# Performance work log

Measured on AMD Instinct MI355X. Metric: run time of the kernel, lower is better.

## Reference

```python
import jax, jax.numpy as jnp
import numpy as np

VOCAB = 50257
EMBED = 512
HEADS = 8
HEAD_DIM = EMBED // HEADS
WINDOW = 128
NUM_CLASS = 20
B, S = 4, 2048


def setup_inputs() -> dict:
    key = jax.random.key(0)
    ks = jax.random.split(key, 16)
    sc = 0.02
    inp = {
        'text': jax.random.randint(ks[0], (B, S), 0, VOCAB),
        'emb': jax.random.normal(ks[1], (VOCAB, EMBED), jnp.float32) * sc,
        'in_w': jax.random.normal(ks[2], (3 * EMBED, EMBED), jnp.float32) * sc,
        'in_b': jnp.zeros((3 * EMBED,), jnp.float32),
        'out_w': jax.random.normal(ks[3], (EMBED, EMBED), jnp.float32) * sc,
        'out_b': jnp.zeros((EMBED,), jnp.float32),
        'w1': jax.random.normal(ks[4], (512, EMBED), jnp.float32) * sc,
        'b1': jnp.zeros((512,), jnp.float32),
        'w2': jax.random.normal(ks[5], (256, 512), jnp.float32) * sc,
        'b2': jnp.zeros((256,), jnp.float32),
        'w3': jax.random.normal(ks[6], (128, 256), jnp.float32) * sc,
        'b3': jnp.zeros((128,), jnp.float32),
        'w4': jax.random.normal(ks[7], (NUM_CLASS, 128), jnp.float32) * sc,
        'b4': jnp.zeros((NUM_CLASS,), jnp.float32),
    }
    return inp


def _banded_mask(seq_len, window):
    i = jnp.arange(seq_len)[:, None]
    j = jnp.arange(seq_len)[None, :]
    allowed = jnp.abs(i - j) <= window  # band of width 2*window+1
    return jnp.where(allowed, 0.0, -jnp.inf).astype(jnp.float32)


def reference(text, emb, in_w, in_b, out_w, out_b, w1, b1, w2, b2, w3, b3, w4, b4):
    # Embedding lookup (dropout is identity in eval mode)
    x = emb[text]  # [B, S, E]
    b, s, e = x.shape

    # torch nn.MultiheadAttention: packed in_proj, scaling by 1/sqrt(head_dim)
    wq, wk, wv = in_w[:e], in_w[e:2 * e], in_w[2 * e:]
    bq, bk, bv = in_b[:e], in_b[e:2 * e], in_b[2 * e:]
    q = (x @ wq.T + bq).reshape(b, s, HEADS, HEAD_DIM)
    k = (x @ wk.T + bk).reshape(b, s, HEADS, HEAD_DIM)
    v = (x @ wv.T + bv).reshape(b, s, HEADS, HEAD_DIM)

    mask = _banded_mask(s, WINDOW)  # [S, S] additive, -inf outside band
    scores = jnp.einsum('bihd,bjhd->bhij', q, k) / jnp.sqrt(jnp.float32(HEAD_DIM))
    probs = jax.nn.softmax(scores + mask, axis=-1)  # [B, H, S, S]
    attn = jnp.einsum('bhij,bjhd->bihd', probs, v).reshape(b, s, e)
    attn = attn @ out_w.T + out_b  # [B, S, E]

    # max-pool over sequence
    ctx = jnp.max(attn, axis=1)  # [B, E]

    # MLP head with leaky_relu (negative_slope=0.01, torch default)
    h = jax.nn.leaky_relu(ctx @ w1.T + b1, 0.01)
    h = jax.nn.leaky_relu(h @ w2.T + b2, 0.01)
    h = jax.nn.leaky_relu(h @ w3.T + b3, 0.01)
    return h @ w4.T + b4  # [B, NUM_CLASS]
```

## Files before the change

kernel.cpp:

```cpp
#include <hip/hip_runtime.h>

typedef unsigned short u16;
typedef __attribute__((ext_vector_type(8))) short bf16x8;
typedef __attribute__((ext_vector_type(4))) float f32x4;

#define S_LEN 2048
#define EMBED 512
#define HEADS 8
#define HDIM 64
#define BATCH 4
#define TOKENS (BATCH * S_LEN)

__device__ __forceinline__ u16 f2bf(float f) {
  union { float f; unsigned u; } v;
  v.f = f;
  unsigned r = v.u + 0x7fffu + ((v.u >> 16) & 1u);
  return (u16)(r >> 16);
}

__device__ __forceinline__ unsigned fkey(float f) {
  unsigned u = __float_as_uint(f);
  return (u & 0x80000000u) ? ~u : (u | 0x80000000u);
}
__device__ __forceinline__ float funkey(unsigned k) {
  unsigned u = (k & 0x80000000u) ? (k ^ 0x80000000u) : ~k;
  return __uint_as_float(u);
}

__device__ __forceinline__ void gl2lds16(const void* g, void* l) {
  __builtin_amdgcn_global_load_lds(
      (const __attribute__((address_space(1))) void*)g,
      (__attribute__((address_space(3))) void*)l, 16, 0, 0);
}

__global__ __launch_bounds__(256) void prep_kernel(
    const int* __restrict__ text, const float* __restrict__ emb,
    const float* __restrict__ in_w, const float* __restrict__ out_w,
    u16* __restrict__ Xb, u16* __restrict__ Wq, u16* __restrict__ Wo,
    unsigned* __restrict__ ctxi) {
  const int bid = blockIdx.x;
  const int tid = threadIdx.x;
  if (bid < 1024) {
    const int t = bid * 8 + (tid >> 5);
    const int c0 = (tid & 31) * 16;
    const float* src = emb + (size_t)text[t] * EMBED + c0;
    u16* dst = Xb + (size_t)t * EMBED + c0;
#pragma unroll
    for (int j = 0; j < 4; ++j) {
      const float4 v = *(const float4*)(src + j * 4);
      dst[j * 4 + 0] = f2bf(v.x); dst[j * 4 + 1] = f2bf(v.y);
      dst[j * 4 + 2] = f2bf(v.z); dst[j * 4 + 3] = f2bf(v.w);
    }
  } else if (bid < 1152) {
    const int wb = bid - 1024;
#pragma unroll
    for (int j = 0; j < 8; ++j) {
      const int idx4 = wb * 2048 + j * 256 + tid;
      const int idx = idx4 * 4;
      const float* src;
      u16* dst;
      if (idx < 1536 * 512) { src = in_w + idx; dst = Wq + idx; }
      else { src = out_w + (idx - 1536 * 512); dst = Wo + (idx - 1536 * 512); }
      const float4 v = *(const float4*)src;
      dst[0] = f2bf(v.x); dst[1] = f2bf(v.y); dst[2] = f2bf(v.z); dst[3] = f2bf(v.w);
    }
  } else {
    for (int i = tid; i < BATCH * EMBED; i += 256) ctxi[i] = 0u;
  }
}

__global__ __launch_bounds__(256, 3) void qkv_mfma(
    const u16* __restrict__ Xb, const u16* __restrict__ Wq,
    const float* __restrict__ in_b,
    u16* __restrict__ qg, u16* __restrict__ kg, u16* __restrict__ vt) {
  __shared__ u16 SM[16384];
  u16* const As = SM;
  u16* const Bs = SM + 8192;
  const int lid = blockIdx.x;
  const int xcd = lid & 7, idx = lid >> 3;
  const int m0 = (xcd * 8 + idx / 12) * 128;
  const int n0 = (idx % 12) * 128;
  const int tid = threadIdx.x;
  const int w = tid >> 6, l = tid & 63, quad = l >> 4, ln = l & 15;
  const int rb = (w >> 1) * 64, cb = (w & 1) * 64;

  f32x4 acc[4][4] = {};

  for (int k0 = 0; k0 < EMBED; k0 += 64) {
#pragma unroll
    for (int it = 0; it < 4; ++it) {
      const int chunk = it * 256 + tid;
      const int row = chunk >> 3, cp = chunk & 7, c = cp ^ (row & 7);
      gl2lds16(Xb + (size_t)(m0 + row) * EMBED + k0 + c * 8, &As[chunk * 8]);
      gl2lds16(Wq + (size_t)(n0 + row) * EMBED + k0 + c * 8, &Bs[chunk * 8]);
    }
    __syncthreads();
#pragma unroll
    for (int s = 0; s < 2; ++s) {
      bf16x8 af[4], bf[4];
#pragma unroll
      for (int i = 0; i < 4; ++i) {
        const int r = rb + 16 * i + ln;
        af[i] = *(const bf16x8*)&As[r * 64 + (((s << 2) + quad) ^ (r & 7)) * 8];
      }
#pragma unroll
      for (int j = 0; j < 4; ++j) {
        const int n = cb + 16 * j + ln;
        bf[j] = *(const bf16x8*)&Bs[n * 64 + (((s << 2) + quad) ^ (n & 7)) * 8];
      }
#pragma unroll
      for (int i = 0; i < 4; ++i)
#pragma unroll
        for (int j = 0; j < 4; ++j)
          acc[i][j] = __builtin_amdgcn_mfma_f32_16x16x32_bf16(af[i], bf[j], acc[i][j], 0, 0, 0);
    }
    __syncthreads();
  }

  const int b = m0 >> 11;
  if (n0 < 1024) {
#pragma unroll
    for (int j = 0; j < 4; ++j) {
      const int n = n0 + cb + 16 * j + ln;
      const float bias = in_b[n];
      const int sec = n >> 9, f = n & 511, h = f >> 6, d = f & 63;
#pragma unroll
      for (int i = 0; i < 4; ++i) {
#pragma unroll
        for (int r = 0; r < 4; ++r) {
          const int t = m0 + rb + 16 * i + quad * 4 + r;
          const int s = t & 2047;
          const float val = acc[i][j][r] + bias;
          if (sec == 0)
            qg[((size_t)((b * HEADS + h) * S_LEN + s)) * HDIM + d] = f2bf(val * 0.125f);
          else
            kg[((size_t)((b * HEADS + h) * S_LEN + s)) * HDIM + d] = f2bf(val);
        }
      }
    }
  } else {
#pragma unroll
    for (int j = 0; j < 4; ++j) {
      const int col = cb + 16 * j + ln;
      const float bias = in_b[n0 + col];
#pragma unroll
      for (int i = 0; i < 4; ++i) {
#pragma unroll
        for (int r = 0; r < 4; ++r) {
          const int row = rb + 16 * i + quad * 4 + r;
          SM[row * 128 + (col ^ (((row >> 3) & 3) << 4))] = f2bf(acc[i][j][r] + bias);
        }
      }
    }
    __syncthreads();
#pragma unroll
    for (int itd = 0; itd < 2; ++itd) {
      const int dl = w * 32 + itd * 16 + ln;
      const int f = (n0 + dl) & 511, h = f >> 6, d = f & 63;
      u16* dst = vt + ((size_t)((b * HEADS + h) * HDIM + d)) * S_LEN + (m0 & 2047);
#pragma unroll
      for (int it2 = 0; it2 < 4; ++it2) {
        const int sb = quad * 8 + it2 * 32;
        const int swc = dl ^ (((sb >> 3) & 3) << 4);
        union { u16 a[8]; bf16x8 v; } u;
#pragma unroll
        for (int k = 0; k < 8; ++k) u.a[k] = SM[(sb + k) * 128 + swc];
        *(bf16x8*)(dst + sb) = u.v;
      }
    }
  }
}

__global__ __launch_bounds__(256, 3) void attn_mfma(
    const u16* __restrict__ qg, const u16* __restrict__ kg,
    const u16* __restrict__ vt, u16* __restrict__ attnb) {
  __shared__ u16 KV[320 * 64];
  __shared__ u16 Pb[4][16 * 40];
  const int lid = blockIdx.x;
  const int nid = (lid & 7) * 128 + (lid >> 3);
  const int bh = nid >> 5;
  const int i0 = (nid & 31) * 64;
  const int jb = i0 - 128;
  const int tid = threadIdx.x;
  const int w = tid >> 6, l = tid & 63, quad = l >> 4, ln = l & 15;

  const u16* qrow = qg + ((size_t)bh * S_LEN + i0 + w * 16 + ln) * HDIM;
  bf16x8 qf[2];
  qf[0] = *(const bf16x8*)(qrow + quad * 8);
  qf[1] = *(const bf16x8*)(qrow + 32 + quad * 8);

  const u16* kbase = kg + (size_t)bh * S_LEN * HDIM;
#pragma unroll
  for (int it = 0; it < 10; ++it) {
    const int chunk = it * 256 + tid;
    const int row = chunk >> 3, cp = chunk & 7, c = cp ^ (row & 7);
    int gj = jb + row;
    gj = gj < 0 ? 0 : (gj > S_LEN - 1 ? S_LEN - 1 : gj);
    gl2lds16(kbase + (size_t)gj * HDIM + c * 8, &KV[chunk * 8]);
  }
  __syncthreads();

  f32x4 sc[18] = {};
#pragma unroll
  for (int jj = 0; jj < 17; ++jj) {
    const int r = (w + jj) * 16 + ln;
    const bf16x8 b0 = *(const bf16x8*)&KV[r * 64 + ((quad) ^ (r & 7)) * 8];
    const bf16x8 b1 = *(const bf16x8*)&KV[r * 64 + ((4 + quad) ^ (r & 7)) * 8];
    f32x4 a = {};
    a = __builtin_amdgcn_mfma_f32_16x16x32_bf16(qf[0], b0, a, 0, 0, 0);
    a = __builtin_amdgcn_mfma_f32_16x16x32_bf16(qf[1], b1, a, 0, 0, 0);
    sc[jj] = a;
  }
  __syncthreads();

  const u16* vbase = vt + (size_t)bh * HDIM * S_LEN;
#pragma unroll
  for (int it = 0; it < 10; ++it) {
    const int chunk = it * 256 + tid;
    const int row = chunk / 40, cp = chunk % 40, c = cp ^ (row & 7);
    int gc = jb + c * 8;
    gc = gc < 0 ? 0 : (gc > S_LEN - 8 ? S_LEN - 8 : gc);
    gl2lds16(vbase + (size_t)row * S_LEN + gc, &KV[chunk * 8]);
  }

  const int q4 = quad * 4;
  float lrow[4] = {0.f, 0.f, 0.f, 0.f};
  const bool interior = (jb >= 0) && (jb + 320 <= S_LEN);
  if (interior) {
#pragma unroll
    for (int jj = 0; jj < 17; ++jj) {
#pragma unroll
      for (int r = 0; r < 4; ++r) {
        const bool valid =
            (jj == 0) ? (q4 + r <= ln) : ((jj == 16) ? (q4 + r >= ln) : true);
        const float e = valid ? __expf(sc[jj][r]) : 0.f;
        sc[jj][r] = e;
        lrow[r] += e;
      }
    }
  } else {
    const int gibase = i0 + w * 16 + q4;
    int lo[4], hi[4];
#pragma unroll
    for (int r = 0; r < 4; ++r) {
      const int gi = gibase + r;
      int lr = gi - 128, hr = gi + 128;
      lo[r] = lr < 0 ? 0 : lr;
      hi[r] = hr > S_LEN - 1 ? S_LEN - 1 : hr;
    }
#pragma unroll
    for (int jj = 0; jj < 17; ++jj) {
      const int gj = jb + (w + jj) * 16 + ln;
#pragma unroll
      for (int r = 0; r < 4; ++r) {
        const bool valid = (gj >= lo[r]) && (gj <= hi[r]);
        const float e = valid ? __expf(sc[jj][r]) : 0.f;
        sc[jj][r] = e;
        lrow[r] += e;
      }
    }
  }
#pragma unroll
  for (int r = 0; r < 4; ++r) {
    lrow[r] += __shfl_xor(lrow[r], 1);
    lrow[r] += __shfl_xor(lrow[r], 2);
    lrow[r] += __shfl_xor(lrow[r], 4);
    lrow[r] += __shfl_xor(lrow[r], 8);
    lrow[r] = 1.0f / lrow[r];
  }

  __syncthreads();

  f32x4 oacc[4] = {};
  u16* pb = &Pb[w][0];
#pragma unroll
  for (int kt = 0; kt < 9; ++kt) {
#pragma unroll
    for (int tt = 0; tt < 2; ++tt) {
      const int s = kt * 2 + tt;
#pragma unroll
      for (int r = 0; r < 4; ++r)
        pb[(q4 + r) * 40 + ln + 16 * tt] = f2bf(sc[s][r]);
    }
    __asm__ volatile("" ::: "memory");
    const bf16x8 pa = *(const bf16x8*)&pb[ln * 40 + quad * 8];
#pragma unroll
    for (int dt = 0; dt < 4; ++dt) {
      const int d = dt * 16 + ln;
      int cc = 2 * w + kt * 4 + quad;
      cc = cc > 39 ? 39 : cc;
      const bf16x8 vb = *(const bf16x8*)&KV[d * 320 + (cc ^ (d & 7)) * 8];
      oacc[dt] = __builtin_amdgcn_mfma_f32_16x16x32_bf16(pa, vb, oacc[dt], 0, 0, 0);
    }
  }

  const int b = bh >> 3, h = bh & 7;
#pragma unroll
  for (int dt = 0; dt < 4; ++dt) {
    const int d = h * HDIM + dt * 16 + ln;
#pragma unroll
    for (int r = 0; r < 4; ++r) {
      const int gi = i0 + w * 16 + q4 + r;
      attnb[((size_t)(b * S_LEN + gi)) * EMBED + d] = f2bf(oacc[dt][r] * lrow[r]);
    }
  }
}

__global__ __launch_bounds__(256, 3) void outproj_mfma(
    const u16* __restrict__ attnb, const u16* __restrict__ Wo,
    const float* __restrict__ out_b, unsigned* __restrict__ ctxi) {
  __shared__ u16 As[128 * 64];
  __shared__ u16 Bs[64 * 64];
  __shared__ float red[4][32];
  const int lid = blockIdx.x;
  const int xcd = lid & 7, idx = lid >> 3;
  const int m0 = (xcd * 8 + (idx >> 3)) * 128;
  const int n0 = (idx & 7) * 64;
  const int tid = threadIdx.x;
  const int w = tid >> 6, l = tid & 63, quad = l >> 4, ln = l & 15;
  const int rb = (w >> 1) * 64, cb = (w & 1) * 32;

  f32x4 acc[4][2] = {};

  for (int k0 = 0; k0 < EMBED; k0 += 64) {
#pragma unroll
    for (int it = 0; it < 4; ++it) {
      const int chunk = it * 256 + tid;
      const int row = chunk >> 3, cp = chunk & 7, c = cp ^ (row & 7);
      gl2lds16(attnb + (size_t)(m0 + row) * EMBED + k0 + c * 8, &As[chunk * 8]);
    }
#pragma unroll
    for (int it = 0; it < 2; ++it) {
      const int chunk = it * 256 + tid;
      const int row = chunk >> 3, cp = chunk & 7, c = cp ^ (row & 7);
      gl2lds16(Wo + (size_t)(n0 + row) * EMBED + k0 + c * 8, &Bs[chunk * 8]);
    }
    __syncthreads();
#pragma unroll
    for (int s = 0; s < 2; ++s) {
      bf16x8 af[4], bf[2];
#pragma unroll
      for (int i = 0; i < 4; ++i) {
        const int r = rb + 16 * i + ln;
        af[i] = *(const bf16x8*)&As[r * 64 + (((s << 2) + quad) ^ (r & 7)) * 8];
      }
#pragma unroll
      for (int j = 0; j < 2; ++j) {
        const int n = cb + 16 * j + ln;
        bf[j] = *(const bf16x8*)&Bs[n * 64 + (((s << 2) + quad) ^ (n & 7)) * 8];
      }
#pragma unroll
      for (int i = 0; i < 4; ++i)
#pragma unroll
        for (int j = 0; j < 2; ++j)
          acc[i][j] = __builtin_amdgcn_mfma_f32_16x16x32_bf16(af[i], bf[j], acc[i][j], 0, 0, 0);
    }
    __syncthreads();
  }

  float cm[2];
#pragma unroll
  for (int j = 0; j < 2; ++j) {
    float m = -1e30f;
#pragma unroll
    for (int i = 0; i < 4; ++i)
#pragma unroll
      for (int r = 0; r < 4; ++r) m = fmaxf(m, acc[i][j][r]);
    m = fmaxf(m, __shfl_xor(m, 16));
    m = fmaxf(m, __shfl_xor(m, 32));
    cm[j] = m;
  }
  if (l < 16) {
#pragma unroll
    for (int j = 0; j < 2; ++j) red[w][16 * j + ln] = cm[j];
  }
  __syncthreads();
  if (tid < 64) {
    const int half = tid >> 5;
    const int cc = tid & 31;
    const float m = fmaxf(red[half][cc], red[half + 2][cc]);
    const int n = n0 + tid;
    const int b = m0 >> 11;
    atomicMax(&ctxi[b * EMBED + n], fkey(m + out_b[n]));
  }
}

__global__ __launch_bounds__(256) void mlp_l1(
    const unsigned* __restrict__ ctxi, const float* __restrict__ w1,
    const float* __restrict__ b1, float* __restrict__ h1g) {
  __shared__ float ctx[512];
  const int b = blockIdx.x >> 5, chunk = blockIdx.x & 31;
  const int tid = threadIdx.x;
  for (int e = tid; e < 512; e += 256) ctx[e] = funkey(ctxi[b * 512 + e]);
  __syncthreads();

  const int og = tid >> 4, ln = tid & 15;
  const int o = chunk * 16 + og;
  const float4* wv = (const float4*)(w1 + (size_t)o * 512 + ln * 32);
  const float4* xv = (const float4*)(ctx + ln * 32);
  float acc = 0.f;
#pragma unroll
  for (int k = 0; k < 8; ++k) {
    const float4 a = wv[k], x = xv[k];
    acc += a.x * x.x + a.y * x.y + a.z * x.z + a.w * x.w;
  }
  acc += __shfl_xor(acc, 1);
  acc += __shfl_xor(acc, 2);
  acc += __shfl_xor(acc, 4);
  acc += __shfl_xor(acc, 8);
  if (ln == 0) {
    const float a = acc + b1[o];
    h1g[b * 512 + o] = a > 0.f ? a : 0.01f * a;
  }
}

__global__ __launch_bounds__(256) void mlp_l2(
    const float* __restrict__ h1g, const float* __restrict__ w2,
    const float* __restrict__ b2, float* __restrict__ h2g) {
  __shared__ float xb[512];
  const int b = blockIdx.x >> 4, chunk = blockIdx.x & 15;
  const int tid = threadIdx.x;
  for (int e = tid; e < 512; e += 256) xb[e] = h1g[b * 512 + e];
  __syncthreads();

  const int og = tid >> 4, ln = tid & 15;
  const int o = chunk * 16 + og;
  const float4* wv = (const float4*)(w2 + (size_t)o * 512 + ln * 32);
  const float4* xv = (const float4*)(xb + ln * 32);
  float acc = 0.f;
#pragma unroll
  for (int k = 0; k < 8; ++k) {
    const float4 a = wv[k], x = xv[k];
    acc += a.x * x.x + a.y * x.y + a.z * x.z + a.w * x.w;
  }
  acc += __shfl_xor(acc, 1);
  acc += __shfl_xor(acc, 2);
  acc += __shfl_xor(acc, 4);
  acc += __shfl_xor(acc, 8);
  if (ln == 0) {
    const float a = acc + b2[o];
    h2g[b * 256 + o] = a > 0.f ? a : 0.01f * a;
  }
}

__global__ __launch_bounds__(256) void mlp_l34(
    const float* __restrict__ h2g,
    const float* __restrict__ w3, const float* __restrict__ b3,
    const float* __restrict__ w4, const float* __restrict__ b4,
    float* __restrict__ out) {
  __shared__ float xb[256], h3[128];
  const int b = blockIdx.x, tid = threadIdx.x;
  if (tid < 256) xb[tid] = h2g[b * 256 + tid];
  __syncthreads();

  {
    const int o = tid >> 1, kh = tid & 1;
    float acc = 0.f;
    const float* wr = w3 + (size_t)o * 256 + kh * 128;
    const float* xr = xb + kh * 128;
    for (int k = 0; k < 128; k += 4) {
      const float4 wv = *(const float4*)(wr + k);
      const float4 xv = *(const float4*)(xr + k);
      acc += wv.x * xv.x + wv.y * xv.y + wv.z * xv.z + wv.w * xv.w;
    }
    acc += __shfl_xor(acc, 1);
    if (kh == 0) { const float a = acc + b3[o]; h3[o] = a > 0.f ? a : 0.01f * a; }
  }
  __syncthreads();

  if (tid < 160) {
    const int o = tid >> 3, ks = tid & 7;
    const float* wr = w4 + (size_t)o * 128 + ks * 16;
    const float* xr = h3 + ks * 16;
    float acc = 0.f;
    for (int k = 0; k < 16; k += 4) {
      const float4 wv = *(const float4*)(wr + k);
      const float4 xv = *(const float4*)(xr + k);
      acc += wv.x * xv.x + wv.y * xv.y + wv.z * xv.z + wv.w * xv.w;
    }
    acc += __shfl_xor(acc, 1);
    acc += __shfl_xor(acc, 2);
    acc += __shfl_xor(acc, 4);
    if (ks == 0) out[b * 20 + o] = acc + b4[o];
  }
}

extern "C" void kernel_launch(void* const* d_in, const int* in_sizes, int n_in,
                              void* d_out, int out_size, void* d_ws, size_t ws_size,
                              hipStream_t stream) {
  (void)in_sizes; (void)n_in; (void)out_size; (void)ws_size;
  const int*   text  = (const int*)d_in[0];
  const float* emb   = (const float*)d_in[1];
  const float* in_w  = (const float*)d_in[2];
  const float* in_b  = (const float*)d_in[3];
  const float* out_w = (const float*)d_in[4];
  const float* out_b = (const float*)d_in[5];
  const float* w1 = (const float*)d_in[6];
  const float* b1 = (const float*)d_in[7];
  const float* w2 = (const float*)d_in[8];
  const float* b2 = (const float*)d_in[9];
  const float* w3 = (const float*)d_in[10];
  const float* b3 = (const float*)d_in[11];
  const float* w4 = (const float*)d_in[12];
  const float* b4 = (const float*)d_in[13];

  char* ws = (char*)d_ws;
  u16* Xb   = (u16*)(ws);
  u16* Wq   = (u16*)(ws + 8388608);
  u16* Wo   = (u16*)(ws + 9961472);
  u16* qg   = (u16*)(ws + 10485760);
  u16* kg   = (u16*)(ws + 18874368);
  u16* vt   = (u16*)(ws + 27262976);
  u16* attn = (u16*)(ws + 35651584);
  unsigned* ctxi = (unsigned*)(ws + 44040192);
  float* h1g  = (float*)(ws + 44048384);
  float* h2g  = (float*)(ws + 44056576);

  prep_kernel<<<1153, 256, 0, stream>>>(text, emb, in_w, out_w, Xb, Wq, Wo, ctxi);
  qkv_mfma<<<768, 256, 0, stream>>>(Xb, Wq, in_b, qg, kg, vt);
  attn_mfma<<<1024, 256, 0, stream>>>(qg, kg, vt, attn);
  outproj_mfma<<<512, 256, 0, stream>>>(attn, Wo, out_b, ctxi);
  mlp_l1<<<128, 256, 0, stream>>>(ctxi, w1, b1, h1g);
  mlp_l2<<<64, 256, 0, stream>>>(h1g, w2, b2, h2g);
  mlp_l34<<<4, 256, 0, stream>>>(h2g, w3, b3, w4, b4, (float*)d_out);
}
```

Baseline: 216.7 us.

## Shrink outproj tile to 64x64 and simplify attention K/V load addressing

The out-projection GEMM moves from 128x64 tiles (each wave computing a 64x32 sub-tile) to 64x64 tiles, where each wave computes a 16x64 strip. This doubles the grid to 1024 blocks and raises the launch-bounds occupancy hint. The attention kernel now skips the index clamping for interior K windows and replaces the per-iteration divide/modulo in the V load with incremental row/column tracking. The smaller tiles give more parallelism and occupancy, but reuse less data per loaded A/B element and emit twice as many atomicMax updates.

```diff
diff --git a/kernel.cpp b/kernel.cpp
--- a/kernel.cpp
+++ b/kernel.cpp
@@ -183,6 +183,7 @@
   const int jb = i0 - 128;
   const int tid = threadIdx.x;
   const int w = tid >> 6, l = tid & 63, quad = l >> 4, ln = l & 15;
+  const bool interior = (jb >= 0) && (jb + 320 <= S_LEN);
 
   const u16* qrow = qg + ((size_t)bh * S_LEN + i0 + w * 16 + ln) * HDIM;
   bf16x8 qf[2];
@@ -190,13 +191,23 @@
   qf[1] = *(const bf16x8*)(qrow + 32 + quad * 8);
 
   const u16* kbase = kg + (size_t)bh * S_LEN * HDIM;
-#pragma unroll
-  for (int it = 0; it < 10; ++it) {
-    const int chunk = it * 256 + tid;
-    const int row = chunk >> 3, cp = chunk & 7, c = cp ^ (row & 7);
-    int gj = jb + row;
-    gj = gj < 0 ? 0 : (gj > S_LEN - 1 ? S_LEN - 1 : gj);
-    gl2lds16(kbase + (size_t)gj * HDIM + c * 8, &KV[chunk * 8]);
+  if (interior) {
+    const u16* kwin = kbase + (size_t)jb * HDIM;
+#pragma unroll
+    for (int it = 0; it < 10; ++it) {
+      const int chunk = it * 256 + tid;
+      const int row = chunk >> 3, cp = chunk & 7, c = cp ^ (row & 7);
+      gl2lds16(kwin + (size_t)row * HDIM + c * 8, &KV[chunk * 8]);
+    }
+  } else {
+#pragma unroll
+    for (int it = 0; it < 10; ++it) {
+      const int chunk = it * 256 + tid;
+      const int row = chunk >> 3, cp = chunk & 7, c = cp ^ (row & 7);
+      int gj = jb + row;
+      gj = gj < 0 ? 0 : (gj > S_LEN - 1 ? S_LEN - 1 : gj);
+      gl2lds16(kbase + (size_t)gj * HDIM + c * 8, &KV[chunk * 8]);
+    }
   }
   __syncthreads();
 
@@ -214,18 +225,28 @@
   __syncthreads();
 
   const u16* vbase = vt + (size_t)bh * HDIM * S_LEN;
-#pragma unroll
-  for (int it = 0; it < 10; ++it) {
-    const int chunk = it * 256 + tid;
-    const int row = chunk / 40, cp = chunk % 40, c = cp ^ (row & 7);
-    int gc = jb + c * 8;
-    gc = gc < 0 ? 0 : (gc > S_LEN - 8 ? S_LEN - 8 : gc);
-    gl2lds16(vbase + (size_t)row * S_LEN + gc, &KV[chunk * 8]);
+  {
+    int row = tid / 40, cp = tid % 40;
+#pragma unroll
+    for (int it = 0; it < 10; ++it) {
+      const int chunk = it * 256 + tid;
+      const int c = cp ^ (row & 7);
+      if (interior) {
+        gl2lds16(vbase + (size_t)row * S_LEN + jb + c * 8, &KV[chunk * 8]);
+      } else {
+        int gc = jb + c * 8;
+        gc = gc < 0 ? 0 : (gc > S_LEN - 8 ? S_LEN - 8 : gc);
+        gl2lds16(vbase + (size_t)row * S_LEN + gc, &KV[chunk * 8]);
+      }
+      cp += 16;
+      const int carry = cp >= 40;
+      cp -= carry ? 40 : 0;
+      row += 6 + carry;
+    }
   }
 
   const int q4 = quad * 4;
   float lrow[4] = {0.f, 0.f, 0.f, 0.f};
-  const bool interior = (jb >= 0) && (jb + 320 <= S_LEN);
   if (interior) {
 #pragma unroll
     for (int jj = 0; jj < 17; ++jj) {
@@ -306,79 +327,53 @@
   }
 }
 
-__global__ __launch_bounds__(256, 3) void outproj_mfma(
+__global__ __launch_bounds__(256, 4) void outproj_mfma(
     const u16* __restrict__ attnb, const u16* __restrict__ Wo,
     const float* __restrict__ out_b, unsigned* __restrict__ ctxi) {
-  __shared__ u16 As[128 * 64];
+  __shared__ u16 As[64 * 64];
   __shared__ u16 Bs[64 * 64];
-  __shared__ float red[4][32];
+  __shared__ float red[4][64];
   const int lid = blockIdx.x;
-  const int xcd = lid & 7, idx = lid >> 3;
-  const int m0 = (xcd * 8 + (idx >> 3)) * 128;
-  const int n0 = (idx & 7) * 64;
+  const int m0 = (lid >> 3) * 64, n0 = (lid & 7) * 64;
   const int tid = threadIdx.x;
   const int w = tid >> 6, l = tid & 63, quad = l >> 4, ln = l & 15;
-  const int rb = (w >> 1) * 64, cb = (w & 1) * 32;
-
-  f32x4 acc[4][2] = {};
+
+  f32x4 acc[4] = {};
 
   for (int k0 = 0; k0 < EMBED; k0 += 64) {
 #pragma unroll
-    for (int it = 0; it < 4; ++it) {
+    for (int it = 0; it < 2; ++it) {
       const int chunk = it * 256 + tid;
       const int row = chunk >> 3, cp = chunk & 7, c = cp ^ (row & 7);
       gl2lds16(attnb + (size_t)(m0 + row) * EMBED + k0 + c * 8, &As[chunk * 8]);
-    }
-#pragma unroll
-    for (int it = 0; it < 2; ++it) {
-      const int chunk = it * 256 + tid;
-      const int row = chunk >> 3, cp = chunk & 7, c = cp ^ (row & 7);
       gl2lds16(Wo + (size_t)(n0 + row) * EMBED + k0 + c * 8, &Bs[chunk * 8]);
     }
     __syncthreads();
 #pragma unroll
     for (int s = 0; s < 2; ++s) {
-      bf16x8 af[4], bf[2];
-#pragma unroll
-      for (int i = 0; i < 4; ++i) {
-        const int r = rb + 16 * i + ln;
-        af[i] = *(const bf16x8*)&As[r * 64 + (((s << 2) + quad) ^ (r & 7)) * 8];
-      }
-#pragma unroll
-      for (int j = 0; j < 2; ++j) {
-        const int n = cb + 16 * j + ln;
-        bf[j] = *(const bf16x8*)&Bs[n * 64 + (((s << 2) + quad) ^ (n & 7)) * 8];
-      }
-#pragma unroll
-      for (int i = 0; i < 4; ++i)
-#pragma unroll
-        for (int j = 0; j < 2; ++j)
-          acc[i][j] = __builtin_amdgcn_mfma_f32_16x16x32_bf16(af[i], bf[j], acc[i][j], 0, 0, 0);
+      const int ar = w * 16 + ln;
+      const bf16x8 af = *(const bf16x8*)&As[ar * 64 + (((s << 2) + quad) ^ (ar & 7)) * 8];
+#pragma unroll
+      for (int j = 0; j < 4; ++j) {
+        const int n = j * 16 + ln;
+        const bf16x8 bf = *(const bf16x8*)&Bs[n * 64 + (((s << 2) + quad) ^ (n & 7)) * 8];
+        acc[j] = __builtin_amdgcn_mfma_f32_16x16x32_bf16(af, bf, acc[j], 0, 0, 0);
+      }
     }
     __syncthreads();
   }
 
-  float cm[2];
-#pragma unroll
-  for (int j = 0; j < 2; ++j) {
-    float m = -1e30f;
-#pragma unroll
-    for (int i = 0; i < 4; ++i)
-#pragma unroll
-      for (int r = 0; r < 4; ++r) m = fmaxf(m, acc[i][j][r]);
+#pragma unroll
+  for (int j = 0; j < 4; ++j) {
+    float m = fmaxf(fmaxf(acc[j][0], acc[j][1]), fmaxf(acc[j][2], acc[j][3]));
     m = fmaxf(m, __shfl_xor(m, 16));
     m = fmaxf(m, __shfl_xor(m, 32));
-    cm[j] = m;
-  }
-  if (l < 16) {
-#pragma unroll
-    for (int j = 0; j < 2; ++j) red[w][16 * j + ln] = cm[j];
+    if (l < 16) red[w][j * 16 + ln] = m;
   }
   __syncthreads();
   if (tid < 64) {
-    const int half = tid >> 5;
-    const int cc = tid & 31;
-    const float m = fmaxf(red[half][cc], red[half + 2][cc]);
+    const float m = fmaxf(fmaxf(red[0][tid], red[1][tid]),
+                          fmaxf(red[2][tid], red[3][tid]));
     const int n = n0 + tid;
     const int b = m0 >> 11;
     atomicMax(&ctxi[b * EMBED + n], fkey(m + out_b[n]));
@@ -519,7 +514,7 @@
   prep_kernel<<<1153, 256, 0, stream>>>(text, emb, in_w, out_w, Xb, Wq, Wo, ctxi);
   qkv_mfma<<<768, 256, 0, stream>>>(Xb, Wq, in_b, qg, kg, vt);
   attn_mfma<<<1024, 256, 0, stream>>>(qg, kg, vt, attn);
-  outproj_mfma<<<512, 256, 0, stream>>>(attn, Wo, out_b, ctxi);
+  outproj_mfma<<<1024, 256, 0, stream>>>(attn, Wo, out_b, ctxi);
   mlp_l1<<<128, 256, 0, stream>>>(ctxi, w1, b1, h1g);
   mlp_l2<<<64, 256, 0, stream>>>(h1g, w2, b2, h2g);
   mlp_l34<<<4, 256, 0, stream>>>(h2g, w3, b3, w4, b4, (float*)d_out);
```

Measured after the change: 220.9 us. Within noise of the previous version (+2.0%).
